# Kernel optimization log

Measured on AMD Instinct MI355X. Metric: run time of the kernel, lower is better.

The kernel has to match this reference:

```python
import jax, jax.numpy as jnp
import numpy as np

TEMPERATURE = 0.07
EPS = 1e-12  # F.normalize default eps

def _l2norm(x):
    n = jnp.linalg.norm(x, axis=1, keepdims=True)
    return x / jnp.maximum(n, EPS)

def setup_inputs() -> dict:
    key = jax.random.key(0)
    k1, k2 = jax.random.split(key)
    N, D = 16384, 256
    return {
        "feat_local": jax.random.normal(k1, (N, D), dtype=jnp.float32),
        "feat_global": jax.random.normal(k2, (N, D), dtype=jnp.float32),
    }

def reference(feat_local, feat_global):
    fl = _l2norm(feat_local)
    fg = _l2norm(feat_global)
    # [N, N] similarity matrix scaled by temperature
    sim = jnp.einsum('nd,md->nm', fl, fg) / TEMPERATURE
    pos_sim = jnp.diagonal(sim)
    loss = -pos_sim + jax.scipy.special.logsumexp(sim, axis=1)
    return loss.mean()
```

## Files before the change

kernel.cpp:

```cpp
#include <hip/hip_runtime.h>
#include <hip/hip_bf16.h>

#define NROWS 16384
#define DIM   256
#define DB    (DIM / 2)
#define SEGS  6
#define BN    128
#define TB    (BN * DB)
#define INVT  14.285714285714286f
#define C1f   20.60992915555662f
#define LN2f  0.6931471805599453f

typedef __attribute__((ext_vector_type(8)))  int   int8v;
typedef __attribute__((ext_vector_type(16))) float f32x16;

#define SCA 0x7F7F7F7Fu
#define SCB 0x7B7B7B7Bu

__device__ __forceinline__ unsigned fp4q(float v) {
    float a = fabsf(v);
    unsigned s = (__float_as_uint(v) >> 28) & 0x8u;
    unsigned idx = (unsigned)(a >= 0.25f) + (a >= 0.75f) + (a >= 1.25f) + (a >= 1.75f)
                 + (a >= 2.5f) + (a >= 3.5f) + (a >= 5.0f);
    return s | idx;
}

__global__ __launch_bounds__(256) void norm_diag_kernel(
    const float* __restrict__ fl, const float* __restrict__ fg,
    unsigned char* __restrict__ A, unsigned char* __restrict__ B,
    float* __restrict__ diag, float* __restrict__ out)
{
    int tid  = threadIdx.x;
    int wave = tid >> 6, lane = tid & 63;
    int row  = blockIdx.x * 4 + wave;
    if (blockIdx.x == 0 && tid == 0) out[0] = 0.0f;

    float4 xl = ((const float4*)(fl + (size_t)row * DIM))[lane];
    float4 xg = ((const float4*)(fg + (size_t)row * DIM))[lane];
    float ssl = xl.x*xl.x + xl.y*xl.y + xl.z*xl.z + xl.w*xl.w;
    float ssg = xg.x*xg.x + xg.y*xg.y + xg.z*xg.z + xg.w*xg.w;
    for (int m = 1; m < 64; m <<= 1) {
        ssl += __shfl_xor(ssl, m, 64);
        ssg += __shfl_xor(ssg, m, 64);
    }
    float il = 1.0f / fmaxf(sqrtf(ssl), 1e-12f);
    float ig = 1.0f / fmaxf(sqrtf(ssg), 1e-12f);
    float nl0 = xl.x*il, nl1 = xl.y*il, nl2 = xl.z*il, nl3 = xl.w*il;
    float ng0 = xg.x*ig, ng1 = xg.y*ig, ng2 = xg.z*ig, ng3 = xg.w*ig;

    unsigned pa4 = fp4q(nl0 * C1f) | (fp4q(nl1 * C1f) << 4)
                 | (fp4q(nl2 * C1f) << 8) | (fp4q(nl3 * C1f) << 12);
    ((unsigned short*)(A + (size_t)row * DB))[lane] = (unsigned short)pa4;

    unsigned pb4 = fp4q(ng0 * 16.0f) | (fp4q(ng1 * 16.0f) << 4)
                 | (fp4q(ng2 * 16.0f) << 8) | (fp4q(ng3 * 16.0f) << 12);
    {
        int kcb4 = lane >> 3;
        unsigned chunk = (unsigned)((row >> 7) * 1024 + ((row >> 6) & 1) * 512
                                    + kcb4 * 64 + (row & 63));
        ((unsigned short*)B)[chunk * 8 + (lane & 7)] = (unsigned short)pb4;
    }

    float d = nl0*ng0 + nl1*ng1 + nl2*ng2 + nl3*ng3;
    for (int m = 1; m < 64; m <<= 1) d += __shfl_xor(d, m, 64);
    if (lane == 0) diag[row] = d;
}

__global__ __launch_bounds__(256, 3) void sim_lse_kernel(
    const unsigned char* __restrict__ A, const unsigned char* __restrict__ B,
    float* __restrict__ lpart)
{
    __shared__ __align__(16) unsigned char bt[2 * TB];

    int tid  = threadIdx.x;
    int lane = tid & 63;
    int l31  = lane & 31, half = lane >> 5;
    int wave = tid >> 6;
    int seg  = blockIdx.x;
    int nt   = 21 + (seg < 2 ? 1 : 0);
    int T0   = seg * 21 + (seg < 2 ? seg : 2);
    int rowBase = blockIdx.y * 128 + wave * 32;

    unsigned vb = (unsigned)(l31 * 16 + half * 1024);

    const int4 zero4 = make_int4(0, 0, 0, 0);

    int8v af[4];
    {
        const unsigned char* ap = A + (size_t)(rowBase + l31) * DB + half * 16;
#pragma unroll
        for (int kk = 0; kk < 4; ++kk) {
            ((int4*)&af[kk])[0] = *(const int4*)(ap + kk * 32);
            ((int4*)&af[kk])[1] = zero4;
        }
    }

    f32x16 lv;
    f32x16 p0, p1, q0, q1;
#pragma unroll
    for (int r = 0; r < 16; ++r) {
        lv[r] = -2.0f;
        q0[r] = 0.0f; q1[r] = 0.0f;
    }

    auto stage = [&](int T, unsigned bufo) {
        const unsigned char* g = B + (size_t)T * TB + (unsigned)tid * 16;
        unsigned lo = bufo + (unsigned)tid * 16;
#pragma unroll
        for (int j = 0; j < 4; ++j) {
            __builtin_amdgcn_global_load_lds(
                (const __attribute__((address_space(1))) unsigned int*)(g + j * 4096),
                (__attribute__((address_space(3))) unsigned int*)&bt[lo + j * 4096],
                16, 0, 0);
        }
    };

#define MFMA4(dst, a, b, cin) \
    dst = __builtin_amdgcn_mfma_scale_f32_32x32x64_f8f6f4(a, b, cin, 4, 4, 0, SCA, 0, SCB)

    auto slot = [&](f32x16& c0, f32x16& c1, f32x16& e0, f32x16& e1,
                    unsigned ab, unsigned offA, unsigned offB) {
#pragma unroll
        for (int r = 0; r < 16; ++r) { c0[r] = 0.0f; c1[r] = 0.0f; }
        int8v b0, b1, b2, b3;
        ((int4*)&b0)[1] = zero4; ((int4*)&b1)[1] = zero4;
        ((int4*)&b2)[1] = zero4; ((int4*)&b3)[1] = zero4;
        ((int4*)&b0)[0] = *(const int4*)&bt[ab + offA];
        ((int4*)&b1)[0] = *(const int4*)&bt[ab + offB];
        MFMA4(c0, af[0], b0, c0);
        MFMA4(c1, af[0], b1, c1);
#pragma unroll
        for (int r = 0; r < 8; ++r)  lv[r] += __builtin_amdgcn_exp2f(e0[r]);
        ((int4*)&b2)[0] = *(const int4*)&bt[ab + offA + 2048u];
        ((int4*)&b3)[0] = *(const int4*)&bt[ab + offB + 2048u];
        MFMA4(c0, af[1], b2, c0);
        MFMA4(c1, af[1], b3, c1);
#pragma unroll
        for (int r = 8; r < 16; ++r) lv[r] += __builtin_amdgcn_exp2f(e0[r]);
        ((int4*)&b0)[0] = *(const int4*)&bt[ab + offA + 4096u];
        ((int4*)&b1)[0] = *(const int4*)&bt[ab + offB + 4096u];
        MFMA4(c0, af[2], b0, c0);
        MFMA4(c1, af[2], b1, c1);
#pragma unroll
        for (int r = 0; r < 8; ++r)  lv[r] += __builtin_amdgcn_exp2f(e1[r]);
        ((int4*)&b2)[0] = *(const int4*)&bt[ab + offA + 6144u];
        ((int4*)&b3)[0] = *(const int4*)&bt[ab + offB + 6144u];
        MFMA4(c0, af[3], b2, c0);
        MFMA4(c1, af[3], b3, c1);
#pragma unroll
        for (int r = 8; r < 16; ++r) lv[r] += __builtin_amdgcn_exp2f(e1[r]);
    };

    stage(T0, 0);

    for (int t = 0; t < nt; ++t) {
        unsigned bufo = (t & 1) ? (unsigned)TB : 0u;
        __syncthreads();

        if (t + 1 < nt)
            stage(T0 + t + 1, (t & 1) ? 0u : (unsigned)TB);

        unsigned ab = vb + bufo;
        slot(p0, p1, q0, q1, ab, 0u,    512u);
        slot(q0, q1, p0, p1, ab, 8192u, 8704u);
    }
#pragma unroll
    for (int r = 0; r < 16; ++r)
        lv[r] += __builtin_amdgcn_exp2f(q0[r]) + __builtin_amdgcn_exp2f(q1[r]);

#pragma unroll
    for (int r = 0; r < 16; ++r) {
        float v = lv[r];
        v += __shfl_xor(v, 1, 64);
        v += __shfl_xor(v, 2, 64);
        v += __shfl_xor(v, 4, 64);
        v += __shfl_xor(v, 8, 64);
        v += __shfl_xor(v, 16, 64);
        lv[r] = v;
    }
    if (l31 == 0) {
#pragma unroll
        for (int r = 0; r < 16; ++r) {
            int row = rowBase + (r & 3) + 8*(r >> 2) + 4*half;
            lpart[(size_t)seg * NROWS + row] = lv[r];
        }
    }
#undef MFMA4
}

__global__ __launch_bounds__(256) void reduce_kernel(
    const float* __restrict__ lpart, const float* __restrict__ diag,
    float* __restrict__ out)
{
    __shared__ float sm[4];
    int gtid = blockIdx.x * 256 + threadIdx.x;
    float s = 0.0f;
    for (int row = gtid; row < NROWS; row += 32 * 256) {
        float t = 0.0f;
#pragma unroll
        for (int g = 0; g < SEGS; ++g) t += lpart[(size_t)g * NROWS + row];
        s += LN2f * log2f(t) - INVT * diag[row];
    }
    for (int m = 1; m < 64; m <<= 1) s += __shfl_xor(s, m, 64);
    int wave = threadIdx.x >> 6, lane = threadIdx.x & 63;
    if (lane == 0) sm[wave] = s;
    __syncthreads();
    if (threadIdx.x == 0) {
        float tot = sm[0] + sm[1] + sm[2] + sm[3];
        atomicAdd(out, tot * (1.0f / NROWS));
    }
}

extern "C" void kernel_launch(void* const* d_in, const int* in_sizes, int n_in,
                              void* d_out, int out_size, void* d_ws, size_t ws_size,
                              hipStream_t stream) {
    const float* fl = (const float*)d_in[0];
    const float* fg = (const float*)d_in[1];
    float* out = (float*)d_out;

    char* ws = (char*)d_ws;
    unsigned char* A = (unsigned char*)ws;
    unsigned char* B = A + (size_t)NROWS * DB;
    float* diag  = (float*)(ws + 2 * (size_t)NROWS * DB);
    float* lpart = diag + NROWS;

    norm_diag_kernel<<<NROWS / 4, 256, 0, stream>>>(fl, fg, A, B, diag, out);
    sim_lse_kernel<<<dim3(SEGS, NROWS / 128), 256, 0, stream>>>(A, B, lpart);
    reduce_kernel<<<32, 256, 0, stream>>>(lpart, diag, out);
}
```

Measured before the change: 122.8 us.

## Fuse normalize, similarity-LSE and reduce into one cooperative kernel

Merges the three kernel launches into a single cooperative kernel that uses grid-wide syncs between the normalize/quantize phase, the MFMA similarity/logsumexp phase and the final reduction. This removes inter-kernel launch gaps and tail effects. In exchange it adds two grid barriers and requires all 768 blocks to be co-resident; otherwise it falls back to the original three-launch path.

```diff
diff --git a/kernel.cpp b/kernel.cpp
--- a/kernel.cpp
+++ b/kernel.cpp
@@ -1,5 +1,8 @@
 #include <hip/hip_runtime.h>
 #include <hip/hip_bf16.h>
+#include <hip/hip_cooperative_groups.h>
+
+namespace cg = cooperative_groups;
 
 #define NROWS 16384
 #define DIM   256
@@ -25,16 +28,12 @@
     return s | idx;
 }
 
-__global__ __launch_bounds__(256) void norm_diag_kernel(
+
+__device__ __forceinline__ void norm_row(
     const float* __restrict__ fl, const float* __restrict__ fg,
     unsigned char* __restrict__ A, unsigned char* __restrict__ B,
-    float* __restrict__ diag, float* __restrict__ out)
-{
-    int tid  = threadIdx.x;
-    int wave = tid >> 6, lane = tid & 63;
-    int row  = blockIdx.x * 4 + wave;
-    if (blockIdx.x == 0 && tid == 0) out[0] = 0.0f;
-
+    float* __restrict__ diag, int row, int lane)
+{
     float4 xl = ((const float4*)(fl + (size_t)row * DIM))[lane];
     float4 xg = ((const float4*)(fg + (size_t)row * DIM))[lane];
     float ssl = xl.x*xl.x + xl.y*xl.y + xl.z*xl.z + xl.w*xl.w;
@@ -54,35 +53,33 @@
 
     unsigned pb4 = fp4q(ng0 * 16.0f) | (fp4q(ng1 * 16.0f) << 4)
                  | (fp4q(ng2 * 16.0f) << 8) | (fp4q(ng3 * 16.0f) << 12);
-    {
-        int kcb4 = lane >> 3;
-        unsigned chunk = (unsigned)((row >> 7) * 1024 + ((row >> 6) & 1) * 512
-                                    + kcb4 * 64 + (row & 63));
-        ((unsigned short*)B)[chunk * 8 + (lane & 7)] = (unsigned short)pb4;
-    }
+    int kcb4 = lane >> 3;
+    unsigned chunk = (unsigned)((row >> 7) * 1024 + ((row >> 6) & 1) * 512
+                                + kcb4 * 64 + (row & 63));
+    ((unsigned short*)B)[chunk * 8 + (lane & 7)] = (unsigned short)pb4;
 
     float d = nl0*ng0 + nl1*ng1 + nl2*ng2 + nl3*ng3;
     for (int m = 1; m < 64; m <<= 1) d += __shfl_xor(d, m, 64);
     if (lane == 0) diag[row] = d;
 }
 
-__global__ __launch_bounds__(256, 3) void sim_lse_kernel(
+#define MFMA4(dst, a, b, cin) \
+    dst = __builtin_amdgcn_mfma_scale_f32_32x32x64_f8f6f4(a, b, cin, 4, 4, 0, SCA, 0, SCB)
+
+__device__ __forceinline__ void sim_phase(
     const unsigned char* __restrict__ A, const unsigned char* __restrict__ B,
-    float* __restrict__ lpart)
-{
-    __shared__ __align__(16) unsigned char bt[2 * TB];
-
-    int tid  = threadIdx.x;
+    float* __restrict__ lpart, unsigned char* bt,
+    int tid, int segX, int blkY)
+{
     int lane = tid & 63;
     int l31  = lane & 31, half = lane >> 5;
     int wave = tid >> 6;
-    int seg  = blockIdx.x;
+    int seg  = segX;
     int nt   = 21 + (seg < 2 ? 1 : 0);
     int T0   = seg * 21 + (seg < 2 ? seg : 2);
-    int rowBase = blockIdx.y * 128 + wave * 32;
+    int rowBase = blkY * 128 + wave * 32;
 
     unsigned vb = (unsigned)(l31 * 16 + half * 1024);
-
     const int4 zero4 = make_int4(0, 0, 0, 0);
 
     int8v af[4];
@@ -114,9 +111,6 @@
                 16, 0, 0);
         }
     };
-
-#define MFMA4(dst, a, b, cin) \
-    dst = __builtin_amdgcn_mfma_scale_f32_32x32x64_f8f6f4(a, b, cin, 4, 4, 0, SCA, 0, SCB)
 
     auto slot = [&](f32x16& c0, f32x16& c1, f32x16& e0, f32x16& e1,
                     unsigned ab, unsigned offA, unsigned offB) {
@@ -185,7 +179,65 @@
             lpart[(size_t)seg * NROWS + row] = lv[r];
         }
     }
-#undef MFMA4
+}
+
+__global__ __launch_bounds__(256, 3) void fused_kernel(
+    const float* __restrict__ fl, const float* __restrict__ fg,
+    unsigned char* __restrict__ A, unsigned char* __restrict__ B,
+    float* __restrict__ diag, float* __restrict__ lpart,
+    float* __restrict__ out)
+{
+    __shared__ __align__(16) unsigned char bt[2 * TB];
+
+    int tid  = threadIdx.x;
+    int lane = tid & 63;
+    int wave = tid >> 6;
+    int bid  = blockIdx.y * gridDim.x + blockIdx.x;
+
+    {
+        int gw = bid * 4 + wave;
+        for (int row = gw; row < NROWS; row += 3072)
+            norm_row(fl, fg, A, B, diag, row, lane);
+    }
+
+    cg::this_grid().sync();
+
+    if (bid == 0 && tid == 0) out[0] = 0.0f;
+
+    sim_phase(A, B, lpart, bt, tid, blockIdx.x, blockIdx.y);
+
+    cg::this_grid().sync();
+
+    if (bid < 64) {
+        int row = bid * 256 + tid;
+        float t = 0.0f;
+#pragma unroll
+        for (int g = 0; g < SEGS; ++g) t += lpart[(size_t)g * NROWS + row];
+        float s = LN2f * log2f(t) - INVT * diag[row];
+        for (int m = 1; m < 64; m <<= 1) s += __shfl_xor(s, m, 64);
+        if (lane == 0) atomicAdd(out, s * (1.0f / NROWS));
+    }
+}
+
+
+__global__ __launch_bounds__(256) void norm_diag_kernel(
+    const float* __restrict__ fl, const float* __restrict__ fg,
+    unsigned char* __restrict__ A, unsigned char* __restrict__ B,
+    float* __restrict__ diag, float* __restrict__ out)
+{
+    int tid  = threadIdx.x;
+    int wave = tid >> 6, lane = tid & 63;
+    int row  = blockIdx.x * 4 + wave;
+    if (blockIdx.x == 0 && tid == 0) out[0] = 0.0f;
+    norm_row(fl, fg, A, B, diag, row, lane);
+}
+
+__global__ __launch_bounds__(256, 3) void sim_lse_kernel(
+    const unsigned char* __restrict__ A, const unsigned char* __restrict__ B,
+    float* __restrict__ lpart)
+{
+    __shared__ __align__(16) unsigned char bt[2 * TB];
+    sim_phase(A, B, lpart, bt, threadIdx.x, blockIdx.x, blockIdx.y);
 }
 
 __global__ __launch_bounds__(256) void reduce_kernel(
@@ -224,7 +276,14 @@
     float* diag  = (float*)(ws + 2 * (size_t)NROWS * DB);
     float* lpart = diag + NROWS;
 
-    norm_diag_kernel<<<NROWS / 4, 256, 0, stream>>>(fl, fg, A, B, diag, out);
-    sim_lse_kernel<<<dim3(SEGS, NROWS / 128), 256, 0, stream>>>(A, B, lpart);
-    reduce_kernel<<<32, 256, 0, stream>>>(lpart, diag, out);
-}
+    void* args[] = { (void*)&fl, (void*)&fg, (void*)&A, (void*)&B,
+                     (void*)&diag, (void*)&lpart, (void*)&out };
+    hipError_t err = hipLaunchCooperativeKernel((const void*)fused_kernel,
+                                                dim3(SEGS, NROWS / 128), dim3(256),
+                                                args, 0, stream);
+    if (err != hipSuccess) {
+        norm_diag_kernel<<<NROWS / 4, 256, 0, stream>>>(fl, fg, A, B, diag, out);
+        sim_lse_kernel<<<dim3(SEGS, NROWS / 128), 256, 0, stream>>>(A, B, lpart);
+        reduce_kernel<<<32, 256, 0, stream>>>(lpart, diag, out);
+    }
+}
```

New measurement: 263.1 us. +114.3%, slower.
